# Optimization experiments

Measured on AMD Instinct MI355X. Metric: run time of the kernel, lower is better.

The kernel has to match this reference:

```python
import jax, jax.numpy as jnp
import numpy as np

B, D, H, W = 16, 384, 64, 64
Dq, Dv, NH, DFF = 768, 384, 12, 1536
EPS = 1e-5


def setup_inputs() -> dict:
    key = jax.random.key(0)
    ks = jax.random.split(key, 8)

    def w(k, out_c, in_c):
        return (jax.random.normal(k, (out_c, in_c), jnp.float32) / np.float32(np.sqrt(in_c)))

    return {
        "x": jax.random.normal(ks[0], (B, D, H, W), jnp.float32),
        "ln1_w": jnp.ones((D, H, W), jnp.float32),
        "ln1_b": jnp.zeros((D, H, W), jnp.float32),
        "qw": w(ks[1], Dq, D), "qb": jnp.zeros((Dq,), jnp.float32),
        "kw": w(ks[2], Dq, D), "kb": jnp.zeros((Dq,), jnp.float32),
        "vw": w(ks[3], Dv, D), "vb": jnp.zeros((Dv,), jnp.float32),
        "hu_w": w(ks[4], D, Dv), "hu_b": jnp.zeros((D,), jnp.float32),
        "ln2_w": jnp.ones((D, H, W), jnp.float32),
        "ln2_b": jnp.zeros((D, H, W), jnp.float32),
        "ff1_w": w(ks[5], DFF, D), "ff1_b": jnp.zeros((DFF,), jnp.float32),
        "ff2_w": w(ks[6], D, DFF), "ff2_b": jnp.zeros((D,), jnp.float32),
    }


def layernorm(x, w, b):
    # torch.nn.LayerNorm((D, H, W)): normalize over last 3 dims, biased var
    mu = x.mean(axis=(1, 2, 3), keepdims=True)
    var = x.var(axis=(1, 2, 3), keepdims=True)
    return (x - mu) * jax.lax.rsqrt(var + EPS) * w + b


def conv1x1(x, w, b):
    # 1x1 conv == channel-mixing matmul; x: (B, Cin, H, W), w: (Cout, Cin)
    return jnp.einsum('bdhw,od->bohw', x, w) + b[None, :, None, None]


def reference(x, ln1_w, ln1_b, qw, qb, kw, kb, vw, vb, hu_w, hu_b,
              ln2_w, ln2_b, ff1_w, ff1_b, ff2_w, ff2_b):
    a = layernorm(x, ln1_w, ln1_b)
    Q = conv1x1(a, qw, qb)  # (B, Dq, H, W)
    K = conv1x1(a, kw, kb)  # (B, Dq, H, W)
    V = conv1x1(a, vw, vb)  # (B, Dv, H, W)

    Q = jax.nn.softmax(Q, axis=1)  # softmax over channels (subtract-max is built in)
    K = jax.nn.softmax(K.reshape(B, Dq, H * W), axis=-1).reshape(B, Dq, H, W)

    Qh = Q.reshape(B, NH, Dq // NH, H, W)
    Kh = K.reshape(B, NH, Dq // NH, H, W)
    Vh = V.reshape(B, NH, Dv // NH, H, W)

    # kernel_size=1: adaptive_avg_pool2d(KV, 1) * 1 == spatial mean of K (x) V,
    # and the grouped 1x1 conv is a per-(batch,head) (Dv/h x Dq/h) matmul on Q.
    KV = jnp.einsum('bhqyx,bhvyx->bhqv', Kh, Vh) / np.float32(H * W)
    QKV = jnp.einsum('bhqv,bhqyx->bhvyx', KV, Qh).reshape(B, Dv, H, W)

    attn = conv1x1(QKV, hu_w, hu_b)  # head unification, (B, D, H, W)
    x = x + attn
    x = layernorm(x, ln2_w, ln2_b)
    ff = conv1x1(jax.nn.gelu(conv1x1(x, ff1_w, ff1_b), approximate=False), ff2_w, ff2_b)
    return x + ff
```

## Files before the change

kernel.cpp:

```cpp
#include <hip/hip_runtime.h>
#include <hip/hip_bf16.h>

using u16 = unsigned short;
typedef __attribute__((ext_vector_type(4))) float f32x4;
typedef __bf16 bf16x8 __attribute__((ext_vector_type(8)));
typedef short s16x4 __attribute__((ext_vector_type(4)));
typedef short s16x8 __attribute__((ext_vector_type(8)));

#define DEVI __device__ __forceinline__

DEVI float b2f(u16 u) {
    union { unsigned i; float f; } x; x.i = ((unsigned)u) << 16; return x.f;
}
DEVI u16 f2b(float f) {
    union { float f; unsigned i; } x; x.f = f;
    unsigned r = (x.i + 0x7fffu + ((x.i >> 16) & 1u)) >> 16;
    return (u16)r;
}

DEVI float gelu_fast(float v) {
    float t = v * (1.5957691f + 0.0713548162f * v * v);
    return v / (1.f + __expf(-t));
}

static constexpr long long PX = 1572864LL;
static constexpr long long PQ = 3145728LL;
static constexpr long long PH = 6291456LL;

DEVI void gl_lds16(const u16* g, u16* l) {
    __builtin_amdgcn_global_load_lds(
        (const __attribute__((address_space(1))) unsigned int*)g,
        (__attribute__((address_space(3))) unsigned int*)l, 16, 0, 0);
}

__global__ __launch_bounds__(256)
void wconv_kernel(const float* __restrict__ qw, const float* __restrict__ kw,
                  const float* __restrict__ vw, const float* __restrict__ huw,
                  const float* __restrict__ ff1w, const float* __restrict__ ff2w,
                  u16* __restrict__ wcv)
{
    int blk = blockIdx.x;
    const float* src; u16* dst; int lb;
    if      (blk < 288)  { src = qw;   dst = wcv;           lb = blk; }
    else if (blk < 576)  { src = kw;   dst = wcv + 294912;  lb = blk - 288; }
    else if (blk < 720)  { src = vw;   dst = wcv + 589824;  lb = blk - 576; }
    else if (blk < 864)  { src = huw;  dst = wcv + 737280;  lb = blk - 720; }
    else if (blk < 1440) { src = ff1w; dst = wcv + 884736;  lb = blk - 864; }
    else                 { src = ff2w; dst = wcv + 1474560; lb = blk - 1440; }
    int i = (lb * 256 + threadIdx.x) * 4;
    f32x4 v = *(const f32x4*)(src + i);
    s16x4 o;
#pragma unroll
    for (int j = 0; j < 4; ++j) o[j] = (short)f2b(v[j]);
    *(s16x4*)(dst + i) = o;
}

__global__ __launch_bounds__(256, 4)
void gemm_bt_kernel(const u16* __restrict__ A, long long strideA,
                    const u16* __restrict__ Bw, long long strideB,
                    const float* __restrict__ bias,
                    u16* __restrict__ C, long long strideC,
                    float* __restrict__ Cf,
                    const u16* __restrict__ addT, long long strideAdd,
                    int K, int N, int doGelu)
{
    const int tid = threadIdx.x;
    const int lane = tid & 63;
    const int wv = tid >> 6;
    const int wr = wv >> 1, wc = wv & 1;
    const int l15 = lane & 15, l4 = lane >> 4;
    const int bm = blockIdx.x, bn = blockIdx.y, bz = blockIdx.z;

    A  += (long long)bz * strideA;
    Bw += (long long)bz * strideB;
    if (C)    C    += (long long)bz * strideC;
    if (Cf)   Cf   += (long long)bz * strideC;
    if (addT) addT += (long long)bz * strideAdd;

    __shared__ u16 lds[2][128 * 64];

    f32x4 acc[4][4] = {};

    auto stage = [&](int kt) {
#pragma unroll
        for (int i = 0; i < 4; ++i) {
            int cid = tid + i * 256;
            int row = cid >> 3, c8 = cid & 7;
            int c8s = c8 ^ (row & 7);
            gl_lds16(A + (long long)(bm * 128 + row) * K + kt + c8s * 8,
                     &lds[0][cid * 8]);
        }
#pragma unroll
        for (int i = 0; i < 4; ++i) {
            int cid = tid + i * 256;
            int row = cid >> 3, c8 = cid & 7;
            int c8s = c8 ^ (row & 7);
            gl_lds16(Bw + (long long)(bn * 128 + row) * K + kt + c8s * 8,
                     &lds[1][cid * 8]);
        }
    };

    auto compute = [&]() {
#pragma unroll
        for (int kk = 0; kk < 2; ++kk) {
            bf16x8 af[4], bfr[4];
#pragma unroll
            for (int mi = 0; mi < 4; ++mi) {
                int row = wr * 64 + mi * 16 + l15;
                int idx8 = (kk * 4 + l4) ^ (row & 7);
                af[mi] = *(const bf16x8*)&lds[0][row * 64 + idx8 * 8];
            }
#pragma unroll
            for (int ni = 0; ni < 4; ++ni) {
                int row = wc * 64 + ni * 16 + l15;
                int idx8 = (kk * 4 + l4) ^ (row & 7);
                bfr[ni] = *(const bf16x8*)&lds[1][row * 64 + idx8 * 8];
            }
#pragma unroll
            for (int mi = 0; mi < 4; ++mi)
#pragma unroll
                for (int ni = 0; ni < 4; ++ni)
                    acc[mi][ni] = __builtin_amdgcn_mfma_f32_16x16x32_bf16(af[mi], bfr[ni], acc[mi][ni], 0, 0, 0);
        }
    };

    stage(0);
    asm volatile("s_waitcnt vmcnt(0)" ::: "memory");
    __syncthreads();
    for (int kt = 64; kt < K; kt += 64) {
        compute();
        __syncthreads();
        stage(kt);
        asm volatile("s_waitcnt vmcnt(0)" ::: "memory");
        __syncthreads();
    }
    compute();

    if (!Cf) {
        u16* st = &lds[0][0];
#pragma unroll
        for (int p = 0; p < 2; ++p) {
            __syncthreads();
            if (wr == p) {
#pragma unroll
                for (int ni = 0; ni < 4; ++ni) {
                    int colL = wc * 64 + ni * 16 + l15;
                    float bv = bias ? bias[bn * 128 + colL] : 0.f;
#pragma unroll
                    for (int mi = 0; mi < 4; ++mi) {
#pragma unroll
                        for (int r = 0; r < 4; ++r) {
                            float v = acc[mi][ni][r] + bv;
                            if (doGelu) v = gelu_fast(v);
                            st[(mi * 16 + l4 * 4 + r) * 136 + colL] = f2b(v);
                        }
                    }
                }
            }
            __syncthreads();
            int lr = tid >> 2, q = tid & 3;
            const u16* src = st + lr * 136 + q * 32;
            u16* dst = C + (long long)(bm * 128 + p * 64 + lr) * N + bn * 128 + q * 32;
#pragma unroll
            for (int j = 0; j < 4; ++j)
                *(s16x8*)(dst + j * 8) = *(const s16x8*)(src + j * 8);
        }
    } else {
        float* stf = (float*)&lds[0][0];
#pragma unroll
        for (int p = 0; p < 4; ++p) {
            __syncthreads();
            if (wc == (p >> 1)) {
#pragma unroll
                for (int nj = 0; nj < 2; ++nj) {
                    int ni = (p & 1) * 2 + nj;
                    int colL = wc * 64 + ni * 16 + l15;
                    int lc = nj * 16 + l15;
                    float bv = bias ? bias[bn * 128 + colL] : 0.f;
#pragma unroll
                    for (int mi = 0; mi < 4; ++mi) {
                        int row0 = wr * 64 + mi * 16 + l4 * 4;
#pragma unroll
                        for (int r = 0; r < 4; ++r) {
                            float v = acc[mi][ni][r] + bv
                                    + b2f(addT[(long long)(bm * 128 + row0 + r) * N + bn * 128 + colL]);
                            stf[lc * 132 + row0 + r] = v;
                        }
                    }
                }
            }
            __syncthreads();
            int lc = tid >> 3, q = tid & 7;
            float* dst = Cf + (long long)(bn * 128 + p * 32 + lc) * 4096 + bm * 128 + q * 16;
            const float* src = stf + lc * 132 + q * 16;
#pragma unroll
            for (int j = 0; j < 4; ++j)
                *(f32x4*)(dst + j * 4) = *(const f32x4*)(src + j * 4);
        }
    }
}

__global__ __launch_bounds__(256)
void stats_part_kernel(const float* __restrict__ x, float* __restrict__ part)
{
    int b = blockIdx.x, cb = blockIdx.y, t = threadIdx.x;
    const float* p = x + (long long)b * PX + (long long)cb * 49152;
    float s = 0.f, q = 0.f;
    for (int i = 0; i < 48; ++i) {
        f32x4 v = *(const f32x4*)(p + (i * 256 + t) * 4);
#pragma unroll
        for (int j = 0; j < 4; ++j) { s += v[j]; q += v[j] * v[j]; }
    }
    for (int off = 32; off; off >>= 1) { s += __shfl_down(s, off); q += __shfl_down(q, off); }
    __shared__ float rs[4], rq[4];
    if ((t & 63) == 0) { rs[t >> 6] = s; rq[t >> 6] = q; }
    __syncthreads();
    if (t == 0) {
        part[(b * 32 + cb) * 2 + 0] = rs[0] + rs[1] + rs[2] + rs[3];
        part[(b * 32 + cb) * 2 + 1] = rq[0] + rq[1] + rq[2] + rq[3];
    }
}

__global__ void stats_fin_kernel(const float* __restrict__ part, float* __restrict__ mu, float* __restrict__ rsg)
{
    int b = blockIdx.x, l = threadIdx.x;
    float s = l < 32 ? part[(b * 32 + l) * 2 + 0] : 0.f;
    float q = l < 32 ? part[(b * 32 + l) * 2 + 1] : 0.f;
    for (int off = 32; off; off >>= 1) { s += __shfl_down(s, off); q += __shfl_down(q, off); }
    if (l == 0) {
        float m = s / 1572864.f;
        float v = q / 1572864.f - m * m; v = fmaxf(v, 0.f);
        mu[b] = m; rsg[b] = rsqrtf(v + 1e-5f);
    }
}

__global__ __launch_bounds__(256)
void ln_apply_T_kernel(const float* __restrict__ src, const float* __restrict__ w, const float* __restrict__ bb,
                       const float* __restrict__ mu, const float* __restrict__ rsg, u16* __restrict__ dstT)
{
    int nt = blockIdx.x, dt = blockIdx.y, b = blockIdx.z;
    int t = threadIdx.x, tx = t & 63, ty = t >> 6;
    __shared__ float tile[64][65];
    float m = mu[b], r = rsg[b];
    const long long base = (long long)b * PX;
#pragma unroll 4
    for (int i = 0; i < 16; ++i) {
        int dy = ty + i * 4;
        int d = dt * 64 + dy, n = nt * 64 + tx;
        long long widx = (long long)d * 4096 + n;
        tile[dy][tx] = (src[base + widx] - m) * r * w[widx] + bb[widx];
    }
    __syncthreads();
#pragma unroll 4
    for (int i = 0; i < 16; ++i) {
        int ny = ty + i * 4;
        int n = nt * 64 + ny, d = dt * 64 + tx;
        dstT[base + (long long)n * 384 + d] = f2b(tile[tx][ny]);
    }
}

__global__ __launch_bounds__(256)
void softmax_rows_kernel(u16* __restrict__ QT)
{
    long long row = (long long)blockIdx.x * 4 + (threadIdx.x >> 6);
    int lane = threadIdx.x & 63;
    u16* p = QT + row * 768;
    float v[12];
#pragma unroll
    for (int g = 0; g < 3; ++g) {
        s16x4 a = *(const s16x4*)(p + g * 256 + lane * 4);
#pragma unroll
        for (int j = 0; j < 4; ++j) v[g * 4 + j] = b2f((u16)a[j]);
    }
    float m = -1e30f;
#pragma unroll
    for (int j = 0; j < 12; ++j) m = fmaxf(m, v[j]);
    for (int off = 32; off; off >>= 1) m = fmaxf(m, __shfl_xor(m, off));
    float s = 0.f;
#pragma unroll
    for (int j = 0; j < 12; ++j) { v[j] = __expf(v[j] - m); s += v[j]; }
    for (int off = 32; off; off >>= 1) s += __shfl_xor(s, off);
    float inv = 1.f / s;
#pragma unroll
    for (int g = 0; g < 3; ++g) {
        s16x4 o;
#pragma unroll
        for (int j = 0; j < 4; ++j) o[j] = (short)f2b(v[g * 4 + j] * inv);
        *(s16x4*)(p + g * 256 + lane * 4) = o;
    }
}

__global__ __launch_bounds__(256)
void kv_part_kernel(const u16* __restrict__ KT, const u16* __restrict__ VT,
                    u16* __restrict__ KVp, float* __restrict__ sp)
{
    const int ch = blockIdx.x, h = blockIdx.y, b = blockIdx.z;
    const int t = threadIdx.x;
    const int lane = t & 63, w = t >> 6;

    __shared__ u16 kraw[128 * 64];
    __shared__ u16 eKT[64 * 128];
    __shared__ u16 Vt[32 * 128];
    __shared__ float reds[4][64];

    const u16* Kp = KT + (long long)b * PQ + (long long)(ch * 128) * 768 + h * 64;
    const u16* Vp = VT + (long long)b * PX + (long long)(ch * 128) * 384 + h * 32;

#pragma unroll
    for (int pass = 0; pass < 4; ++pass) {
        int cid = t + pass * 256;
        int row = cid >> 3, c8 = cid & 7;
        gl_lds16(Kp + (long long)row * 768 + c8 * 8, kraw + cid * 8);
    }

    {
        int v0 = (t & 7) * 4;
#pragma unroll
        for (int pass = 0; pass < 4; ++pass) {
            int n = (t >> 3) + pass * 32;
            s16x4 v4 = *(const s16x4*)(Vp + (long long)n * 384 + v0);
#pragma unroll
            for (int j = 0; j < 4; ++j) {
                int row = v0 + j;
                Vt[row * 128 + (n ^ ((row & 7) << 3))] = (u16)v4[j];
            }
        }
    }

    asm volatile("s_waitcnt vmcnt(0)" ::: "memory");
    __syncthreads();

    const int c = lane;
    {
        float s = 0.f;
        const int swz = (c & 7) << 3;
#pragma unroll
        for (int r8 = 0; r8 < 4; ++r8) {
            int rbase = w * 32 + r8 * 8;
            s16x8 buf;
#pragma unroll
            for (int j = 0; j < 8; ++j) {
                float e = __expf(b2f(kraw[(rbase + j) * 64 + c]));
                s += e;
                buf[j] = (short)f2b(e);
            }
            *(s16x8*)&eKT[c * 128 + (rbase ^ swz)] = buf;
        }
        reds[w][c] = s;
    }
    __syncthreads();

    if (t < 64)
        sp[((long long)(b * 12 + h) * 32 + ch) * 64 + t] =
            reds[0][t] + reds[1][t] + reds[2][t] + reds[3][t];

    const int l15 = lane & 15, l4 = lane >> 4;
    const int qrow = w * 16 + l15;
    const int sa = (qrow & 7) << 3;
    const int v0row = l15, v1row = 16 + l15;
    const int s0 = (v0row & 7) << 3, s1 = (v1row & 7) << 3;
    f32x4 acc0 = {}, acc1 = {};
#pragma unroll
    for (int ns = 0; ns < 4; ++ns) {
        int na = ns * 32 + l4 * 8;
        bf16x8 a  = *(const bf16x8*)&eKT[qrow * 128 + (na ^ sa)];
        bf16x8 b0 = *(const bf16x8*)&Vt[v0row * 128 + (na ^ s0)];
        bf16x8 b1 = *(const bf16x8*)&Vt[v1row * 128 + (na ^ s1)];
        acc0 = __builtin_amdgcn_mfma_f32_16x16x32_bf16(a, b0, acc0, 0, 0, 0);
        acc1 = __builtin_amdgcn_mfma_f32_16x16x32_bf16(a, b1, acc1, 0, 0, 0);
    }
    u16* Kb = KVp + ((long long)(b * 12 + h) * 32 + ch) * 2048;
#pragma unroll
    for (int r = 0; r < 4; ++r) {
        int q = w * 16 + l4 * 4 + r;
        Kb[q * 32 + l15]      = f2b(acc0[r]);
        Kb[q * 32 + 16 + l15] = f2b(acc1[r]);
    }
}

__global__ __launch_bounds__(256)
void kv_fin_kernel(const u16* __restrict__ KVp, const float* __restrict__ sp,
                   u16* __restrict__ WeffT)
{
    const int h = blockIdx.x, b = blockIdx.y;
    const int t = threadIdx.x;
    __shared__ float fac[64];
    __shared__ float kvt[32][64];

    const long long pb = (long long)(b * 12 + h) * 32;
    if (t < 64) {
        float s = 0.f;
#pragma unroll
        for (int ch = 0; ch < 32; ++ch) s += sp[(pb + ch) * 64 + t];
        fac[t] = 1.f / (s * 4096.f);
    }
    __syncthreads();

    const int v0 = (t & 3) * 8, q = t >> 2;
    float acc[8] = {};
#pragma unroll
    for (int ch = 0; ch < 32; ++ch) {
        s16x8 kv8 = *(const s16x8*)&KVp[(pb + ch) * 2048 + q * 32 + v0];
#pragma unroll
        for (int j = 0; j < 8; ++j) acc[j] += b2f((u16)kv8[j]);
    }
    float fq = fac[q];
#pragma unroll
    for (int j = 0; j < 8; ++j) kvt[v0 + j][q] = acc[j] * fq;
    __syncthreads();

    u16* Wb = WeffT + (long long)b * 294912;
    for (int i = t; i < 64 * 384; i += 256) {
        int qq = i / 384, cc = i % 384;
        int cv = cc - h * 32;
        float val = (cv >= 0 && cv < 32) ? kvt[cv][qq] : 0.f;
        Wb[(long long)(h * 64 + qq) * 384 + cc] = f2b(val);
    }
}

__global__ __launch_bounds__(256)
void wtrans_kernel(const float* __restrict__ w, const float* __restrict__ bb,
                   u16* __restrict__ wT, u16* __restrict__ bT)
{
    int nt = blockIdx.x, dt = blockIdx.y;
    const float* src = blockIdx.z ? bb : w;
    u16* dst = blockIdx.z ? bT : wT;
    int t = threadIdx.x, tx = t & 63, ty = t >> 6;
    __shared__ float tile[64][65];
#pragma unroll 4
    for (int i = 0; i < 16; ++i) {
        int dy = ty + i * 4;
        tile[dy][tx] = src[(long long)(dt * 64 + dy) * 4096 + nt * 64 + tx];
    }
    __syncthreads();
#pragma unroll 4
    for (int i = 0; i < 16; ++i) {
        int ny = ty + i * 4;
        dst[(long long)(nt * 64 + ny) * 384 + dt * 64 + tx] = f2b(tile[tx][ny]);
    }
}

__global__ __launch_bounds__(256)
void resid1T_kernel(const float* __restrict__ x, const u16* __restrict__ attnT,
                    u16* __restrict__ sT, float* __restrict__ part2)
{
    int nt = blockIdx.x, dt = blockIdx.y, b = blockIdx.z;
    int t = threadIdx.x, tx = t & 63, ty = t >> 6;
    __shared__ float tile[64][65];
    const long long base = (long long)b * PX;
#pragma unroll 4
    for (int i = 0; i < 16; ++i) {
        int dy = ty + i * 4;
        tile[dy][tx] = x[base + (long long)(dt * 64 + dy) * 4096 + nt * 64 + tx];
    }
    __syncthreads();
    float ps = 0.f, pq = 0.f;
#pragma unroll 4
    for (int i = 0; i < 16; ++i) {
        int ny = ty + i * 4;
        long long idx = base + (long long)(nt * 64 + ny) * 384 + dt * 64 + tx;
        float val = tile[tx][ny] + b2f(attnT[idx]);
        sT[idx] = f2b(val);
        ps += val; pq += val * val;
    }
    for (int off = 32; off; off >>= 1) { ps += __shfl_down(ps, off); pq += __shfl_down(pq, off); }
    __shared__ float rs[4], rq[4];
    if ((t & 63) == 0) { rs[t >> 6] = ps; rq[t >> 6] = pq; }
    __syncthreads();
    if (t == 0) {
        int bid = (b * 6 + dt) * 64 + nt;
        part2[bid * 2 + 0] = rs[0] + rs[1] + rs[2] + rs[3];
        part2[bid * 2 + 1] = rq[0] + rq[1] + rq[2] + rq[3];
    }
}

__global__ __launch_bounds__(256)
void stats_fin2_kernel(const float* __restrict__ part2, float* __restrict__ mu, float* __restrict__ rsg)
{
    int b = blockIdx.x, t = threadIdx.x;
    float s = 0.f, q = 0.f;
    for (int i = t; i < 384; i += 256) { s += part2[(b * 384 + i) * 2]; q += part2[(b * 384 + i) * 2 + 1]; }
    for (int off = 32; off; off >>= 1) { s += __shfl_down(s, off); q += __shfl_down(q, off); }
    __shared__ float rs[4], rq[4];
    if ((t & 63) == 0) { rs[t >> 6] = s; rq[t >> 6] = q; }
    __syncthreads();
    if (t == 0) {
        float S = rs[0] + rs[1] + rs[2] + rs[3], Q = rq[0] + rq[1] + rq[2] + rq[3];
        float m = S / 1572864.f;
        float v = Q / 1572864.f - m * m; v = fmaxf(v, 0.f);
        mu[b] = m; rsg[b] = rsqrtf(v + 1e-5f);
    }
}

__global__ __launch_bounds__(256)
void ln2_apply_kernel(const u16* __restrict__ sT, const u16* __restrict__ wT, const u16* __restrict__ bT,
                      const float* __restrict__ mu, const float* __restrict__ rsg, u16* __restrict__ x2T)
{
    int blk = blockIdx.x, b = blockIdx.y, t = threadIdx.x;
    float m = mu[b], r = rsg[b];
    long long wi = (long long)blk * 2048 + t * 8;
    long long gi = (long long)b * PX + wi;
    s16x8 sv = *(const s16x8*)(sT + gi);
    s16x8 wv = *(const s16x8*)(wT + wi);
    s16x8 bv = *(const s16x8*)(bT + wi);
    s16x8 o;
#pragma unroll
    for (int j = 0; j < 8; ++j)
        o[j] = (short)f2b((b2f((u16)sv[j]) - m) * r * b2f((u16)wv[j]) + b2f((u16)bv[j]));
    *(s16x8*)(x2T + gi) = o;
}

extern "C" void kernel_launch(void* const* d_in, const int* in_sizes, int n_in,
                              void* d_out, int out_size, void* d_ws, size_t ws_size,
                              hipStream_t stream)
{
    const float* x    = (const float*)d_in[0];
    const float* ln1w = (const float*)d_in[1];
    const float* ln1b = (const float*)d_in[2];
    const float* qw   = (const float*)d_in[3];
    const float* qb   = (const float*)d_in[4];
    const float* kw   = (const float*)d_in[5];
    const float* kb   = (const float*)d_in[6];
    const float* vw   = (const float*)d_in[7];
    const float* vb   = (const float*)d_in[8];
    const float* huw  = (const float*)d_in[9];
    const float* hub  = (const float*)d_in[10];
    const float* ln2w = (const float*)d_in[11];
    const float* ln2b = (const float*)d_in[12];
    const float* ff1w = (const float*)d_in[13];
    const float* ff1b = (const float*)d_in[14];
    const float* ff2w = (const float*)d_in[15];
    const float* ff2b = (const float*)d_in[16];
    float* out = (float*)d_out;

    char* ws = (char*)d_ws;
    u16*   aT    = (u16*)(ws + 0);
    u16*   QT    = (u16*)(ws + 50331648LL);
    u16*   KT    = (u16*)(ws + 150994944LL);
    u16*   VT    = (u16*)(ws + 251658240LL);
    u16*   WeffT = (u16*)(ws + 301989888LL);
    u16*   wcv   = (u16*)(ws + 311427072LL);
    float* fbuf  = (float*)(ws + 315555840LL);

    u16*   KVp    = (u16*)(ws + 0);
    float* sp     = (float*)(ws + 25165824LL);
    u16*   WcombB = (u16*)(ws + 27525120LL);

    u16* sT = KT;
    u16* wT = (u16*)(ws + 150994944LL + 50331648LL);
    u16* bT = (u16*)(ws + 150994944LL + 53477376LL);
    u16* g8 = KT;

    u16* x2T   = QT;
    u16* attnT = VT;

    u16* qwB   = wcv;
    u16* kwB   = wcv + 294912;
    u16* vwB   = wcv + 589824;
    u16* huwB  = wcv + 737280;
    u16* ff1wB = wcv + 884736;
    u16* ff2wB = wcv + 1474560;

    float* part1 = fbuf;
    float* mu1   = fbuf + 1024;
    float* rs1   = fbuf + 1040;
    float* part2 = fbuf + 1056;
    float* mu2   = part2 + 12288;
    float* rs2   = mu2 + 16;

    wconv_kernel<<<2016, 256, 0, stream>>>(qw, kw, vw, huw, ff1w, ff2w, wcv);

    stats_part_kernel<<<dim3(16, 32), 256, 0, stream>>>(x, part1);
    stats_fin_kernel<<<16, 64, 0, stream>>>(part1, mu1, rs1);
    ln_apply_T_kernel<<<dim3(64, 6, 16), 256, 0, stream>>>(x, ln1w, ln1b, mu1, rs1, aT);

    gemm_bt_kernel<<<dim3(32, 6, 16), 256, 0, stream>>>(aT, PX, qwB, 0, qb, QT, PQ, nullptr, nullptr, 0, 384, 768, 0);
    gemm_bt_kernel<<<dim3(32, 6, 16), 256, 0, stream>>>(aT, PX, kwB, 0, kb, KT, PQ, nullptr, nullptr, 0, 384, 768, 0);
    gemm_bt_kernel<<<dim3(32, 3, 16), 256, 0, stream>>>(aT, PX, vwB, 0, vb, VT, PX, nullptr, nullptr, 0, 384, 384, 0);

    softmax_rows_kernel<<<16384, 256, 0, stream>>>(QT);

    kv_part_kernel<<<dim3(32, 12, 16), 256, 0, stream>>>(KT, VT, KVp, sp);
    kv_fin_kernel<<<dim3(12, 16), 256, 0, stream>>>(KVp, sp, WeffT);

    wtrans_kernel<<<dim3(64, 6, 2), 256, 0, stream>>>(ln2w, ln2b, wT, bT);

    gemm_bt_kernel<<<dim3(3, 6, 16), 256, 0, stream>>>(huwB, 0, WeffT, 294912, nullptr, WcombB, 294912, nullptr, nullptr, 0, 384, 768, 0);

    gemm_bt_kernel<<<dim3(32, 3, 16), 256, 0, stream>>>(QT, PQ, WcombB, 294912, hub, attnT, PX, nullptr, nullptr, 0, 768, 384, 0);

    resid1T_kernel<<<dim3(64, 6, 16), 256, 0, stream>>>(x, attnT, sT, part2);
    stats_fin2_kernel<<<16, 256, 0, stream>>>(part2, mu2, rs2);
    ln2_apply_kernel<<<dim3(768, 16), 256, 0, stream>>>(sT, wT, bT, mu2, rs2, x2T);

    for (int c = 0; c < 2; ++c) {
        gemm_bt_kernel<<<dim3(32, 12, 8), 256, 0, stream>>>(
            x2T + (long long)c * 8 * PX, PX, ff1wB, 0, ff1b,
            g8, PH, nullptr, nullptr, 0, 384, 1536, 1);
        gemm_bt_kernel<<<dim3(32, 3, 8), 256, 0, stream>>>(
            g8, PH, ff2wB, 0, ff2b,
            nullptr, PX, out + (long long)c * 8 * PX,
            x2T + (long long)c * 8 * PX, PX, 1536, 384, 0);
    }
}
```

Baseline: 777.7 us.

## Add 128x256-tile 512-thread GEMM kernel for Q, K and FF1 projections

```diff
diff --git a/kernel.cpp b/kernel.cpp
--- a/kernel.cpp
+++ b/kernel.cpp
@@ -53,6 +53,114 @@
 #pragma unroll
     for (int j = 0; j < 4; ++j) o[j] = (short)f2b(v[j]);
     *(s16x4*)(dst + i) = o;
+}
+
+__global__ __launch_bounds__(512, 6)
+void gemm_wide_kernel(const u16* __restrict__ A, long long strideA,
+                      const u16* __restrict__ Bw,
+                      const float* __restrict__ bias,
+                      u16* __restrict__ C, long long strideC,
+                      int K, int N, int doGelu)
+{
+    const int tid = threadIdx.x;
+    const int lane = tid & 63;
+    const int w = tid >> 6;
+    const int wr = w >> 2, wc = w & 3;
+    const int l15 = lane & 15, l4 = lane >> 4;
+    const int bm = blockIdx.x, bn = blockIdx.y, bz = blockIdx.z;
+
+    A += (long long)bz * strideA;
+    C += (long long)bz * strideC;
+
+    __shared__ u16 lds[128 * 64 + 256 * 64];
+    u16* ldsA = lds;
+    u16* ldsB = lds + 128 * 64;
+
+    f32x4 acc[4][4] = {};
+
+    auto stage = [&](int kt) {
+#pragma unroll
+        for (int i = 0; i < 2; ++i) {
+            int cid = tid + i * 512;
+            int row = cid >> 3, c8 = cid & 7;
+            int c8s = c8 ^ (row & 7);
+            gl_lds16(A + (long long)(bm * 128 + row) * K + kt + c8s * 8,
+                     &ldsA[cid * 8]);
+        }
+#pragma unroll
+        for (int i = 0; i < 4; ++i) {
+            int cid = tid + i * 512;
+            int row = cid >> 3, c8 = cid & 7;
+            int c8s = c8 ^ (row & 7);
+            gl_lds16(Bw + (long long)(bn * 256 + row) * K + kt + c8s * 8,
+                     &ldsB[cid * 8]);
+        }
+    };
+
+    auto compute = [&]() {
+#pragma unroll
+        for (int kk = 0; kk < 2; ++kk) {
+            bf16x8 af[4], bfr[4];
+#pragma unroll
+            for (int mi = 0; mi < 4; ++mi) {
+                int row = wr * 64 + mi * 16 + l15;
+                int idx8 = (kk * 4 + l4) ^ (row & 7);
+                af[mi] = *(const bf16x8*)&ldsA[row * 64 + idx8 * 8];
+            }
+#pragma unroll
+            for (int ni = 0; ni < 4; ++ni) {
+                int row = wc * 64 + ni * 16 + l15;
+                int idx8 = (kk * 4 + l4) ^ (row & 7);
+                bfr[ni] = *(const bf16x8*)&ldsB[row * 64 + idx8 * 8];
+            }
+#pragma unroll
+            for (int mi = 0; mi < 4; ++mi)
+#pragma unroll
+                for (int ni = 0; ni < 4; ++ni)
+                    acc[mi][ni] = __builtin_amdgcn_mfma_f32_16x16x32_bf16(af[mi], bfr[ni], acc[mi][ni], 0, 0, 0);
+        }
+    };
+
+    stage(0);
+    asm volatile("s_waitcnt vmcnt(0)" ::: "memory");
+    __syncthreads();
+    for (int kt = 64; kt < K; kt += 64) {
+        compute();
+        __syncthreads();
+        stage(kt);
+        asm volatile("s_waitcnt vmcnt(0)" ::: "memory");
+        __syncthreads();
+    }
+    compute();
+
+    u16* st = lds;
+#pragma unroll
+    for (int p = 0; p < 4; ++p) {
+        int rp = p >> 1, cp = p & 1;
+        __syncthreads();
+        if (wr == rp && (wc >> 1) == cp) {
+#pragma unroll
+            for (int ni = 0; ni < 4; ++ni) {
+                int colL = (wc & 1) * 64 + ni * 16 + l15;
+                float bv = bias ? bias[bn * 256 + cp * 128 + colL] : 0.f;
+#pragma unroll
+                for (int mi = 0; mi < 4; ++mi) {
+#pragma unroll
+                    for (int r = 0; r < 4; ++r) {
+                        float v = acc[mi][ni][r] + bv;
+                        if (doGelu) v = gelu_fast(v);
+                        st[(mi * 16 + l4 * 4 + r) * 136 + colL] = f2b(v);
+                    }
+                }
+            }
+        }
+        __syncthreads();
+        int lr = tid >> 3, q = tid & 7;
+        const u16* src = st + lr * 136 + q * 16;
+        u16* dst = C + (long long)(bm * 128 + rp * 64 + lr) * N + bn * 256 + cp * 128 + q * 16;
+        *(s16x8*)(dst)     = *(const s16x8*)(src);
+        *(s16x8*)(dst + 8) = *(const s16x8*)(src + 8);
+    }
 }
 
 __global__ __launch_bounds__(256, 4)
@@ -574,8 +682,8 @@
     stats_fin_kernel<<<16, 64, 0, stream>>>(part1, mu1, rs1);
     ln_apply_T_kernel<<<dim3(64, 6, 16), 256, 0, stream>>>(x, ln1w, ln1b, mu1, rs1, aT);
 
-    gemm_bt_kernel<<<dim3(32, 6, 16), 256, 0, stream>>>(aT, PX, qwB, 0, qb, QT, PQ, nullptr, nullptr, 0, 384, 768, 0);
-    gemm_bt_kernel<<<dim3(32, 6, 16), 256, 0, stream>>>(aT, PX, kwB, 0, kb, KT, PQ, nullptr, nullptr, 0, 384, 768, 0);
+    gemm_wide_kernel<<<dim3(32, 3, 16), 512, 0, stream>>>(aT, PX, qwB, qb, QT, PQ, 384, 768, 0);
+    gemm_wide_kernel<<<dim3(32, 3, 16), 512, 0, stream>>>(aT, PX, kwB, kb, KT, PQ, 384, 768, 0);
     gemm_bt_kernel<<<dim3(32, 3, 16), 256, 0, stream>>>(aT, PX, vwB, 0, vb, VT, PX, nullptr, nullptr, 0, 384, 384, 0);
 
     softmax_rows_kernel<<<16384, 256, 0, stream>>>(QT);
@@ -594,9 +702,9 @@
     ln2_apply_kernel<<<dim3(768, 16), 256, 0, stream>>>(sT, wT, bT, mu2, rs2, x2T);
 
     for (int c = 0; c < 2; ++c) {
-        gemm_bt_kernel<<<dim3(32, 12, 8), 256, 0, stream>>>(
-            x2T + (long long)c * 8 * PX, PX, ff1wB, 0, ff1b,
-            g8, PH, nullptr, nullptr, 0, 384, 1536, 1);
+        gemm_wide_kernel<<<dim3(32, 6, 8), 512, 0, stream>>>(
+            x2T + (long long)c * 8 * PX, PX, ff1wB, ff1b,
+            g8, PH, 384, 1536, 1);
         gemm_bt_kernel<<<dim3(32, 3, 8), 256, 0, stream>>>(
             g8, PH, ff2wB, 0, ff2b,
             nullptr, PX, out + (long long)c * 8 * PX,
```

Measured after the change: 1.536 ms. 1.98x slower.
